# Kernel tuning notes

Hardware: AMD Instinct MI355X
Metric: run time of the kernel (lower is better)

## Reference

```python
import jax, jax.numpy as jnp
import numpy as np

B = 1048576
L = 4   # latent_dim
F = 4   # f_dim
H = 32  # hidden width


def setup_inputs() -> dict:
    key = jax.random.key(0)
    ks = jax.random.split(key, 10)
    z = jax.random.normal(ks[0], (B, L, F), jnp.float32)
    z_int = jax.random.normal(ks[1], (B, L, F), jnp.float32)
    mask = jax.random.randint(ks[2], (L, L), 0, 2, jnp.int32)
    I = jax.random.randint(ks[3], (B, 1, L), 0, 2, jnp.int32)
    W1 = jax.random.normal(ks[4], (L * F, H), jnp.float32) * (1.0 / np.sqrt(L * F))
    b1 = jnp.zeros((H,), jnp.float32)
    W2 = jax.random.normal(ks[5], (H, H), jnp.float32) * (1.0 / np.sqrt(H))
    b2 = jnp.zeros((H,), jnp.float32)
    W3 = jax.random.normal(ks[6], (H, F), jnp.float32) * (1.0 / np.sqrt(H))
    b3 = jnp.zeros((F,), jnp.float32)
    return dict(z=z, z_int=z_int, W1=W1, b1=b1, W2=W2, b2=b2, W3=W3, b3=b3,
                mask=mask, I=I)


def reference(z, z_int, W1, b1, W2, b2, W3, b3, mask, I):
    # NOTE: in the original torch code, the I-conditional writes are always
    # overwritten by the subsequent column assignment, so I and z_int do not
    # affect the output (dead code, faithfully reproduced).
    Bn = z.shape[0]
    maskf = mask.astype(z.dtype)
    cols = maskf.T                                   # [L, L], row i == mask[:, i]
    # (z * mask[:, i]) broadcasts mask[:, i] over z's LAST dim, as in torch.
    masked = (z[None, :, :, :] * cols[:, None, None, :]).reshape(L, Bn, L * F)
    h = jax.nn.relu(jnp.einsum('ibk,kh->ibh', masked, W1) + b1)
    h = jax.nn.relu(jnp.einsum('ibh,hm->ibm', h, W2) + b2)
    out_net = jnp.einsum('ibm,mf->ibf', h, W3) + b3  # [L, B, F]
    # one eps vector of shape [F] per column i, broadcast over batch
    eps = jax.random.normal(jax.random.key(42), (L, F), z.dtype)
    out_net = out_net + eps[:, None, :]
    cond = jnp.any(mask == 1, axis=0)                # [L]: `1 in mask[:, i]`
    zt = jnp.swapaxes(z, 0, 1)                       # [L, B, F]
    out = jnp.where(cond[:, None, None], out_net, zt)
    return jnp.swapaxes(out, 0, 1)                   # [B, L, F]
```

## Files before the change

### kernel.cpp

```cpp
#include <hip/hip_runtime.h>
#include <cmath>
#include <cstdint>
#include <cstring>


static inline uint32_t rotl32(uint32_t v, int r) { return (v << r) | (v >> (32 - r)); }

static void threefry2x32_42(uint32_t x0, uint32_t x1, uint32_t& o0, uint32_t& o1) {
    const uint32_t k0 = 0u, k1 = 42u;
    const uint32_t ks[3] = { k0, k1, k0 ^ k1 ^ 0x1BD11BDAu };
    static const int R[8] = { 13, 15, 26, 6, 17, 29, 16, 24 };
    x0 += ks[0];
    x1 += ks[1];
    for (int g = 1; g <= 5; ++g) {
        const int* rr = &R[((g - 1) & 1) * 4];
        for (int j = 0; j < 4; ++j) {
            x0 += x1;
            x1 = rotl32(x1, rr[j]);
            x1 ^= x0;
        }
        x0 += ks[g % 3];
        x1 += ks[(g + 1) % 3] + (uint32_t)g;
    }
    o0 = x0;
    o1 = x1;
}

static double erfinv_d(double x) {
    float xf = (float)x;
    float w = -logf((1.0f - xf) * (1.0f + xf));
    float p;
    if (w < 5.0f) {
        w -= 2.5f;
        p = 2.81022636e-08f;
        p = fmaf(p, w, 3.43273939e-07f);
        p = fmaf(p, w, -3.5233877e-06f);
        p = fmaf(p, w, -4.39150654e-06f);
        p = fmaf(p, w, 0.00021858087f);
        p = fmaf(p, w, -0.00125372503f);
        p = fmaf(p, w, -0.00417768164f);
        p = fmaf(p, w, 0.246640727f);
        p = fmaf(p, w, 1.50140941f);
    } else {
        w = sqrtf(w) - 3.0f;
        p = -0.000200214257f;
        p = fmaf(p, w, 0.000100950558f);
        p = fmaf(p, w, 0.00134934322f);
        p = fmaf(p, w, -0.00367342844f);
        p = fmaf(p, w, 0.00573950773f);
        p = fmaf(p, w, -0.0076224613f);
        p = fmaf(p, w, 0.00943887047f);
        p = fmaf(p, w, 1.00167406f);
        p = fmaf(p, w, 2.83297682f);
    }
    double y = (double)(p * xf);
    const double c = 1.1283791670955126;
    for (int it = 0; it < 3; ++it) {
        double err = erf(y) - x;
        y -= err / (c * exp(-y * y));
    }
    return y;
}

struct EpsT { float e[16]; };

static void compute_eps(float* e) {
    const float lo = -0.99999994f;
    for (int i = 0; i < 16; ++i) {
        uint32_t a, b;
        threefry2x32_42(0u, (uint32_t)i, a, b);
        uint32_t bits = a ^ b;
        uint32_t fb = (bits >> 9) | 0x3f800000u;
        float f;
        memcpy(&f, &fb, 4);
        float u = f - 1.0f;
        float v = u * 2.0f + lo;
        if (v < lo) v = lo;
        e[i] = (float)(sqrt(2.0) * erfinv_d((double)v));
    }
}


typedef _Float16 half8 __attribute__((ext_vector_type(8)));
typedef __fp16  fp16x2 __attribute__((ext_vector_type(2)));
typedef __fp16  fp16x4 __attribute__((ext_vector_type(4)));
typedef __fp16  fp16x8 __attribute__((ext_vector_type(8)));
typedef uint32_t uint32x4 __attribute__((ext_vector_type(4)));
typedef float floatx4 __attribute__((ext_vector_type(4)));
typedef float floatx16 __attribute__((ext_vector_type(16)));

static __device__ inline half8 pack8_relu(float a0, float a1, float a2, float a3,
                                          float a4, float a5, float a6, float a7) {
    fp16x2 p0 = __builtin_amdgcn_cvt_pkrtz(a0, a1);
    fp16x2 p1 = __builtin_amdgcn_cvt_pkrtz(a2, a3);
    fp16x2 p2 = __builtin_amdgcn_cvt_pkrtz(a4, a5);
    fp16x2 p3 = __builtin_amdgcn_cvt_pkrtz(a6, a7);
    fp16x4 q0 = __builtin_shufflevector(p0, p1, 0, 1, 2, 3);
    fp16x4 q1 = __builtin_shufflevector(p2, p3, 0, 1, 2, 3);
    fp16x8 r  = __builtin_shufflevector(q0, q1, 0, 1, 2, 3, 4, 5, 6, 7);
    const fp16x8 z8 = (fp16x8)0;
    r = __builtin_elementwise_max(r, z8);
    return __builtin_bit_cast(half8, r);
}

__global__ __launch_bounds__(256, 3) void scm_mfma(
    const float* __restrict__ z,
    const float* __restrict__ W1, const float* __restrict__ b1,
    const float* __restrict__ W2, const float* __restrict__ b2,
    const float* __restrict__ W3, const float* __restrict__ b3,
    const int* __restrict__ mask,
    float* __restrict__ out, EpsT ep, int B)
{
    const int lane = threadIdx.x & 63;
    const int hv   = lane >> 5;
    const int n    = lane & 31;
    const int wid  = blockIdx.x * (blockDim.x >> 6) + (threadIdx.x >> 6);
    const int nw   = gridDim.x * (blockDim.x >> 6);
    const int T    = B >> 5;

    int mku[16];
#pragma unroll
    for (int t = 0; t < 16; ++t) mku[t] = __builtin_amdgcn_readfirstlane(mask[t]);
    int cond[4];
    uint32_t M01[4], M23[4];
#pragma unroll
    for (int i = 0; i < 4; ++i) {
        cond[i] = mku[i] | mku[4 + i] | mku[8 + i] | mku[12 + i];
        M01[i] = (mku[i]      ? 0x0000FFFFu : 0u) | (mku[4 + i]  ? 0xFFFF0000u : 0u);
        M23[i] = (mku[8 + i]  ? 0x0000FFFFu : 0u) | (mku[12 + i] ? 0xFFFF0000u : 0u);
    }

    half8 w1, w2f[2], w3f[2];
#pragma unroll
    for (int j = 0; j < 8; ++j)
        w1[j] = (_Float16)W1[(hv * 8 + j) * 32 + n];
    const uint32x4 w1u = __builtin_bit_cast(uint32x4, w1);
    half8 w1m[4];
#pragma unroll
    for (int i = 0; i < 4; ++i) {
        uint32x4 wm;
        wm.x = w1u.x & M01[i];
        wm.y = w1u.y & M23[i];
        wm.z = w1u.z & M01[i];
        wm.w = w1u.w & M23[i];
        w1m[i] = __builtin_bit_cast(half8, wm);
    }
#pragma unroll
    for (int q = 0; q < 2; ++q)
#pragma unroll
        for (int j = 0; j < 8; ++j) {
            const int row = 16 * q + 4 * hv + 8 * (j >> 2) + (j & 3);
            w2f[q][j] = (_Float16)W2[row * 32 + n];
            w3f[q][j] = (n < 8) ? (_Float16)W3[row * 4 + (n & 3)] : (_Float16)0.f;
        }

    floatx16 b1v, b2v;
#pragma unroll
    for (int r = 0; r < 16; ++r) {
        const int h = (r & 3) + 8 * (r >> 2) + 4 * hv;
        b1v[r] = b1[h];
        b2v[r] = b2[h];
    }
    float eb[8];
#pragma unroll
    for (int s2 = 0; s2 < 2; ++s2)
#pragma unroll
        for (int f = 0; f < 4; ++f)
            eb[s2 * 4 + f] = b3[f] + ep.e[(2 * hv + s2) * 4 + f] - b2v[f];

    int t = wid;
    floatx4 za = { 0.f, 0.f, 0.f, 0.f }, zb = za;
    if (t < T) {
        const floatx4* p = reinterpret_cast<const floatx4*>(z + ((size_t)t * 32 + n) * 16) + hv * 2;
        za = p[0]; zb = p[1];
    }
    while (t < T) {
        const int tn = t + nw;
        floatx4 na = { 0.f, 0.f, 0.f, 0.f }, nb = na;
        if (tn < T) {
            const floatx4* p = reinterpret_cast<const floatx4*>(z + ((size_t)tn * 32 + n) * 16) + hv * 2;
            na = p[0]; nb = p[1];
        }

        half8 bz;
        bz[0] = (_Float16)za.x; bz[1] = (_Float16)za.y;
        bz[2] = (_Float16)za.z; bz[3] = (_Float16)za.w;
        bz[4] = (_Float16)zb.x; bz[5] = (_Float16)zb.y;
        bz[6] = (_Float16)zb.z; bz[7] = (_Float16)zb.w;

        float ov[8];
        ov[0] = za.x; ov[1] = za.y; ov[2] = za.z; ov[3] = za.w;
        ov[4] = zb.x; ov[5] = zb.y; ov[6] = zb.z; ov[7] = zb.w;

#pragma unroll
        for (int p2 = 0; p2 < 2; ++p2) {
            const int iA = 2 * p2, iB = 2 * p2 + 1;
            floatx16 cA = __builtin_amdgcn_mfma_f32_32x32x16_f16(w1m[iA], bz, b1v, 0, 0, 0);
            floatx16 cB = __builtin_amdgcn_mfma_f32_32x32x16_f16(w1m[iB], bz, b1v, 0, 0, 0);
            half8 paA = pack8_relu(cA[0], cA[1], cA[2], cA[3], cA[4], cA[5], cA[6], cA[7]);
            half8 pbA = pack8_relu(cA[8], cA[9], cA[10], cA[11], cA[12], cA[13], cA[14], cA[15]);
            half8 paB = pack8_relu(cB[0], cB[1], cB[2], cB[3], cB[4], cB[5], cB[6], cB[7]);
            half8 pbB = pack8_relu(cB[8], cB[9], cB[10], cB[11], cB[12], cB[13], cB[14], cB[15]);
            floatx16 dA = __builtin_amdgcn_mfma_f32_32x32x16_f16(w2f[0], paA, b2v, 0, 0, 0);
            floatx16 dB = __builtin_amdgcn_mfma_f32_32x32x16_f16(w2f[0], paB, b2v, 0, 0, 0);
            dA = __builtin_amdgcn_mfma_f32_32x32x16_f16(w2f[1], pbA, dA, 0, 0, 0);
            dB = __builtin_amdgcn_mfma_f32_32x32x16_f16(w2f[1], pbB, dB, 0, 0, 0);
            half8 qaA = pack8_relu(dA[0], dA[1], dA[2], dA[3], dA[4], dA[5], dA[6], dA[7]);
            half8 qbA = pack8_relu(dA[8], dA[9], dA[10], dA[11], dA[12], dA[13], dA[14], dA[15]);
            half8 qaB = pack8_relu(dB[0], dB[1], dB[2], dB[3], dB[4], dB[5], dB[6], dB[7]);
            half8 qbB = pack8_relu(dB[8], dB[9], dB[10], dB[11], dB[12], dB[13], dB[14], dB[15]);
            floatx16 eA = __builtin_amdgcn_mfma_f32_32x32x16_f16(w3f[0], qaA, b2v, 0, 0, 0);
            floatx16 eB = __builtin_amdgcn_mfma_f32_32x32x16_f16(w3f[0], qaB, b2v, 0, 0, 0);
            eA = __builtin_amdgcn_mfma_f32_32x32x16_f16(w3f[1], qbA, eA, 0, 0, 0);
            eB = __builtin_amdgcn_mfma_f32_32x32x16_f16(w3f[1], qbB, eB, 0, 0, 0);

            const bool ow  = (p2 == hv);
            const bool wrA = ow && (cond[iA] != 0);
            const bool wrB = ow && (cond[iB] != 0);
#pragma unroll
            for (int f = 0; f < 4; ++f) {
                const float vA = eA[f] + eb[f];
                const float vB = eB[f] + eb[4 + f];
                ov[f]     = wrA ? vA : ov[f];
                ov[4 + f] = wrB ? vB : ov[4 + f];
            }
        }

        floatx4* op = reinterpret_cast<floatx4*>(out + ((size_t)t * 32 + n) * 16 + hv * 8);
        floatx4 o0 = { ov[0], ov[1], ov[2], ov[3] };
        floatx4 o1 = { ov[4], ov[5], ov[6], ov[7] };
        op[0] = o0;
        op[1] = o1;

        t = tn; za = na; zb = nb;
    }
}

extern "C" void kernel_launch(void* const* d_in, const int* in_sizes, int n_in,
                              void* d_out, int out_size, void* d_ws, size_t ws_size,
                              hipStream_t stream) {
    const float* z  = (const float*)d_in[0];
    const float* W1 = (const float*)d_in[2];
    const float* b1 = (const float*)d_in[3];
    const float* W2 = (const float*)d_in[4];
    const float* b2 = (const float*)d_in[5];
    const float* W3 = (const float*)d_in[6];
    const float* b3 = (const float*)d_in[7];
    const int* mask = (const int*)d_in[8];
    float* out = (float*)d_out;

    const int B = in_sizes[0] / 16;

    EpsT ep;
    compute_eps(ep.e);

    dim3 grid(768), block(256);
    hipLaunchKernelGGL(scm_mfma, grid, block, 0, stream,
                       z, W1, b1, W2, b2, W3, b3, mask, out, ep, B);
}
```

Before: 184.2 us.

## Split each 32-row tile across two wavefronts, halving per-wave MLP passes

Each wavefront now handles only two of the four mask columns for a tile, and a pair of waves shares one 32-sample tile. The K-dimension of z is rotated so each half-wave's output columns sit in the first four B-operand slots, so one store per lane is enough. This halves the per-wave MFMA chain and register footprint, which lets occupancy rise to 4 blocks per SIMD with a larger grid. The cost is that each z tile is loaded twice from memory or cache, once per wave in the pair.

```diff
diff --git a/kernel.cpp b/kernel.cpp
--- a/kernel.cpp
+++ b/kernel.cpp
@@ -103,7 +103,7 @@
     return __builtin_bit_cast(half8, r);
 }
 
-__global__ __launch_bounds__(256, 3) void scm_mfma(
+__global__ __launch_bounds__(256, 4) void scm_mfma(
     const float* __restrict__ z,
     const float* __restrict__ W1, const float* __restrict__ b1,
     const float* __restrict__ W2, const float* __restrict__ b2,
@@ -116,7 +116,9 @@
     const int n    = lane & 31;
     const int wid  = blockIdx.x * (blockDim.x >> 6) + (threadIdx.x >> 6);
     const int nw   = gridDim.x * (blockDim.x >> 6);
+    const int rl   = wid & 1;
     const int T    = B >> 5;
+    const int ts   = nw >> 1;
 
     int mku[16];
 #pragma unroll
@@ -129,22 +131,26 @@
         M01[i] = (mku[i]      ? 0x0000FFFFu : 0u) | (mku[4 + i]  ? 0xFFFF0000u : 0u);
         M23[i] = (mku[8 + i]  ? 0x0000FFFFu : 0u) | (mku[12 + i] ? 0xFFFF0000u : 0u);
     }
+    const int      condA = rl ? cond[2] : cond[0];
+    const int      condB = rl ? cond[3] : cond[1];
+    const uint32_t M01A  = rl ? M01[2] : M01[0], M23A = rl ? M23[2] : M23[0];
+    const uint32_t M01B  = rl ? M01[3] : M01[1], M23B = rl ? M23[3] : M23[1];
+
+    const int base0 = 8 * rl + 4 * hv;
+    const int base1 = (base0 + 8) & 15;
 
     half8 w1, w2f[2], w3f[2];
 #pragma unroll
-    for (int j = 0; j < 8; ++j)
-        w1[j] = (_Float16)W1[(hv * 8 + j) * 32 + n];
+    for (int j = 0; j < 4; ++j) {
+        w1[j]     = (_Float16)W1[(base0 + j) * 32 + n];
+        w1[4 + j] = (_Float16)W1[(base1 + j) * 32 + n];
+    }
     const uint32x4 w1u = __builtin_bit_cast(uint32x4, w1);
-    half8 w1m[4];
-#pragma unroll
-    for (int i = 0; i < 4; ++i) {
-        uint32x4 wm;
-        wm.x = w1u.x & M01[i];
-        wm.y = w1u.y & M23[i];
-        wm.z = w1u.z & M01[i];
-        wm.w = w1u.w & M23[i];
-        w1m[i] = __builtin_bit_cast(half8, wm);
-    }
+    uint32x4 wmA, wmB;
+    wmA.x = w1u.x & M01A; wmA.y = w1u.y & M23A; wmA.z = w1u.z & M01A; wmA.w = w1u.w & M23A;
+    wmB.x = w1u.x & M01B; wmB.y = w1u.y & M23B; wmB.z = w1u.z & M01B; wmB.w = w1u.w & M23B;
+    const half8 w1mA = __builtin_bit_cast(half8, wmA);
+    const half8 w1mB = __builtin_bit_cast(half8, wmB);
 #pragma unroll
     for (int q = 0; q < 2; ++q)
 #pragma unroll
@@ -161,25 +167,28 @@
         b1v[r] = b1[h];
         b2v[r] = b2[h];
     }
-    float eb[8];
-#pragma unroll
-    for (int s2 = 0; s2 < 2; ++s2)
-#pragma unroll
-        for (int f = 0; f < 4; ++f)
-            eb[s2 * 4 + f] = b3[f] + ep.e[(2 * hv + s2) * 4 + f] - b2v[f];
-
-    int t = wid;
+    float eb[4];
+#pragma unroll
+    for (int f = 0; f < 4; ++f) {
+        const float eA = rl ? ep.e[8 + f]  : ep.e[f];
+        const float eB = rl ? ep.e[12 + f] : ep.e[4 + f];
+        eb[f] = b3[f] + (hv ? eB : eA) - b2v[f];
+    }
+
+    int t = wid >> 1;
     floatx4 za = { 0.f, 0.f, 0.f, 0.f }, zb = za;
     if (t < T) {
-        const floatx4* p = reinterpret_cast<const floatx4*>(z + ((size_t)t * 32 + n) * 16) + hv * 2;
-        za = p[0]; zb = p[1];
+        const float* zr = z + ((size_t)t * 32 + n) * 16;
+        za = *reinterpret_cast<const floatx4*>(zr + base0);
+        zb = *reinterpret_cast<const floatx4*>(zr + base1);
     }
     while (t < T) {
-        const int tn = t + nw;
+        const int tn = t + ts;
         floatx4 na = { 0.f, 0.f, 0.f, 0.f }, nb = na;
         if (tn < T) {
-            const floatx4* p = reinterpret_cast<const floatx4*>(z + ((size_t)tn * 32 + n) * 16) + hv * 2;
-            na = p[0]; nb = p[1];
+            const float* zr = z + ((size_t)tn * 32 + n) * 16;
+            na = *reinterpret_cast<const floatx4*>(zr + base0);
+            nb = *reinterpret_cast<const floatx4*>(zr + base1);
         }
 
         half8 bz;
@@ -188,49 +197,34 @@
         bz[4] = (_Float16)zb.x; bz[5] = (_Float16)zb.y;
         bz[6] = (_Float16)zb.z; bz[7] = (_Float16)zb.w;
 
-        float ov[8];
-        ov[0] = za.x; ov[1] = za.y; ov[2] = za.z; ov[3] = za.w;
-        ov[4] = zb.x; ov[5] = zb.y; ov[6] = zb.z; ov[7] = zb.w;
-
-#pragma unroll
-        for (int p2 = 0; p2 < 2; ++p2) {
-            const int iA = 2 * p2, iB = 2 * p2 + 1;
-            floatx16 cA = __builtin_amdgcn_mfma_f32_32x32x16_f16(w1m[iA], bz, b1v, 0, 0, 0);
-            floatx16 cB = __builtin_amdgcn_mfma_f32_32x32x16_f16(w1m[iB], bz, b1v, 0, 0, 0);
-            half8 paA = pack8_relu(cA[0], cA[1], cA[2], cA[3], cA[4], cA[5], cA[6], cA[7]);
-            half8 pbA = pack8_relu(cA[8], cA[9], cA[10], cA[11], cA[12], cA[13], cA[14], cA[15]);
-            half8 paB = pack8_relu(cB[0], cB[1], cB[2], cB[3], cB[4], cB[5], cB[6], cB[7]);
-            half8 pbB = pack8_relu(cB[8], cB[9], cB[10], cB[11], cB[12], cB[13], cB[14], cB[15]);
-            floatx16 dA = __builtin_amdgcn_mfma_f32_32x32x16_f16(w2f[0], paA, b2v, 0, 0, 0);
-            floatx16 dB = __builtin_amdgcn_mfma_f32_32x32x16_f16(w2f[0], paB, b2v, 0, 0, 0);
-            dA = __builtin_amdgcn_mfma_f32_32x32x16_f16(w2f[1], pbA, dA, 0, 0, 0);
-            dB = __builtin_amdgcn_mfma_f32_32x32x16_f16(w2f[1], pbB, dB, 0, 0, 0);
-            half8 qaA = pack8_relu(dA[0], dA[1], dA[2], dA[3], dA[4], dA[5], dA[6], dA[7]);
-            half8 qbA = pack8_relu(dA[8], dA[9], dA[10], dA[11], dA[12], dA[13], dA[14], dA[15]);
-            half8 qaB = pack8_relu(dB[0], dB[1], dB[2], dB[3], dB[4], dB[5], dB[6], dB[7]);
-            half8 qbB = pack8_relu(dB[8], dB[9], dB[10], dB[11], dB[12], dB[13], dB[14], dB[15]);
-            floatx16 eA = __builtin_amdgcn_mfma_f32_32x32x16_f16(w3f[0], qaA, b2v, 0, 0, 0);
-            floatx16 eB = __builtin_amdgcn_mfma_f32_32x32x16_f16(w3f[0], qaB, b2v, 0, 0, 0);
-            eA = __builtin_amdgcn_mfma_f32_32x32x16_f16(w3f[1], qbA, eA, 0, 0, 0);
-            eB = __builtin_amdgcn_mfma_f32_32x32x16_f16(w3f[1], qbB, eB, 0, 0, 0);
-
-            const bool ow  = (p2 == hv);
-            const bool wrA = ow && (cond[iA] != 0);
-            const bool wrB = ow && (cond[iB] != 0);
-#pragma unroll
-            for (int f = 0; f < 4; ++f) {
-                const float vA = eA[f] + eb[f];
-                const float vB = eB[f] + eb[4 + f];
-                ov[f]     = wrA ? vA : ov[f];
-                ov[4 + f] = wrB ? vB : ov[4 + f];
-            }
-        }
-
-        floatx4* op = reinterpret_cast<floatx4*>(out + ((size_t)t * 32 + n) * 16 + hv * 8);
-        floatx4 o0 = { ov[0], ov[1], ov[2], ov[3] };
-        floatx4 o1 = { ov[4], ov[5], ov[6], ov[7] };
-        op[0] = o0;
-        op[1] = o1;
+        floatx16 cA = __builtin_amdgcn_mfma_f32_32x32x16_f16(w1mA, bz, b1v, 0, 0, 0);
+        floatx16 cB = __builtin_amdgcn_mfma_f32_32x32x16_f16(w1mB, bz, b1v, 0, 0, 0);
+        half8 paA = pack8_relu(cA[0], cA[1], cA[2], cA[3], cA[4], cA[5], cA[6], cA[7]);
+        half8 pbA = pack8_relu(cA[8], cA[9], cA[10], cA[11], cA[12], cA[13], cA[14], cA[15]);
+        half8 paB = pack8_relu(cB[0], cB[1], cB[2], cB[3], cB[4], cB[5], cB[6], cB[7]);
+        half8 pbB = pack8_relu(cB[8], cB[9], cB[10], cB[11], cB[12], cB[13], cB[14], cB[15]);
+        floatx16 dA = __builtin_amdgcn_mfma_f32_32x32x16_f16(w2f[0], paA, b2v, 0, 0, 0);
+        floatx16 dB = __builtin_amdgcn_mfma_f32_32x32x16_f16(w2f[0], paB, b2v, 0, 0, 0);
+        dA = __builtin_amdgcn_mfma_f32_32x32x16_f16(w2f[1], pbA, dA, 0, 0, 0);
+        dB = __builtin_amdgcn_mfma_f32_32x32x16_f16(w2f[1], pbB, dB, 0, 0, 0);
+        half8 qaA = pack8_relu(dA[0], dA[1], dA[2], dA[3], dA[4], dA[5], dA[6], dA[7]);
+        half8 qbA = pack8_relu(dA[8], dA[9], dA[10], dA[11], dA[12], dA[13], dA[14], dA[15]);
+        half8 qaB = pack8_relu(dB[0], dB[1], dB[2], dB[3], dB[4], dB[5], dB[6], dB[7]);
+        half8 qbB = pack8_relu(dB[8], dB[9], dB[10], dB[11], dB[12], dB[13], dB[14], dB[15]);
+        floatx16 eA = __builtin_amdgcn_mfma_f32_32x32x16_f16(w3f[0], qaA, b2v, 0, 0, 0);
+        floatx16 eB = __builtin_amdgcn_mfma_f32_32x32x16_f16(w3f[0], qaB, b2v, 0, 0, 0);
+        eA = __builtin_amdgcn_mfma_f32_32x32x16_f16(w3f[1], qbA, eA, 0, 0, 0);
+        eB = __builtin_amdgcn_mfma_f32_32x32x16_f16(w3f[1], qbB, eB, 0, 0, 0);
+
+        const bool wr = (hv ? condB : condA) != 0;
+        floatx4 ov;
+#pragma unroll
+        for (int f = 0; f < 4; ++f) {
+            const float vv = (hv ? eB[f] : eA[f]) + eb[f];
+            ov[f] = wr ? vv : za[f];
+        }
+
+        *reinterpret_cast<floatx4*>(out + ((size_t)t * 32 + n) * 16 + base0) = ov;
 
         t = tn; za = na; zb = nb;
     }
@@ -254,7 +248,7 @@
     EpsT ep;
     compute_eps(ep.e);
 
-    dim3 grid(768), block(256);
+    dim3 grid(1024), block(256);
     hipLaunchKernelGGL(scm_mfma, grid, block, 0, stream,
                        z, W1, b1, W2, b2, W3, b3, mask, out, ep, B);
 }
```

After: 194.6 us. +5.7%, slower.
